# Kernel tuning notes

Measured on AMD Instinct MI355X. Metric: run time of the kernel, lower is better.

## Reference

```python
import jax, jax.numpy as jnp
import numpy as np

N_NODES = 10000
N_EDGES = 640000
DIM = 128


def setup_inputs() -> dict:
    key = jax.random.key(0)
    ks = jax.random.split(key, 10)
    s = 1.0 / np.sqrt(DIM)
    return {
        "x": jax.random.normal(ks[0], (N_NODES, DIM), dtype=jnp.float32),
        "edge_index": jax.random.randint(ks[1], (2, N_EDGES), 0, N_NODES, dtype=jnp.int64),
        "fc_w": jax.random.normal(ks[2], (DIM, DIM), dtype=jnp.float32) * s,
        "fc_b": jax.random.normal(ks[3], (DIM,), dtype=jnp.float32) * s,
        "f_lw": jax.random.normal(ks[4], (DIM, DIM), dtype=jnp.float32) * s,
        "f_lb": jax.random.normal(ks[5], (DIM,), dtype=jnp.float32) * s,
        "f_rw": jax.random.normal(ks[6], (DIM, DIM), dtype=jnp.float32) * s,
        "n_lw": jax.random.normal(ks[7], (DIM, DIM), dtype=jnp.float32) * s,
        "n_lb": jax.random.normal(ks[8], (DIM,), dtype=jnp.float32) * s,
        "n_rw": jax.random.normal(ks[9], (DIM, DIM), dtype=jnp.float32) * s,
    }


def _sage_conv(h, src, dst, lw, lb, rw, n_nodes):
    # mean aggregation of source-node features at target nodes
    msg = h[src]                                                   # [E, D]
    summed = jax.ops.segment_sum(msg, dst, num_segments=n_nodes)   # [N, D]
    cnt = jax.ops.segment_sum(jnp.ones_like(dst, dtype=h.dtype), dst, num_segments=n_nodes)
    agg = summed / jnp.maximum(cnt, 1.0)[:, None]
    # PyG SAGEConv: lin_l(agg) + lin_r(x); lin_l has bias, lin_r does not
    return agg @ lw.T + lb + h @ rw.T


def reference(x, edge_index, fc_w, fc_b, f_lw, f_lb, f_rw, n_lw, n_lb, n_rw):
    n_nodes = x.shape[0]
    src, dst = edge_index[0], edge_index[1]
    inp = x @ fc_w.T + fc_b                                        # fc residual branch
    h = jax.nn.relu(_sage_conv(x, src, dst, f_lw, f_lb, f_rw, n_nodes))
    # dropout(p=0.3) is identity in eval mode
    h = _sage_conv(h, src, dst, n_lw, n_lb, n_rw, n_nodes)
    return jax.nn.relu(h + inp)
```

## Files before the change

### kernel.cpp

```cpp
#include <hip/hip_runtime.h>
#include <hip/hip_fp8.h>

#define NN 10000
#define NE 640000
#define DIM 128
#define NB 157
#define REGCAP 4608
#define MT1 157
#define EPB 4096
#define G_FILL 157
#define NODECAP 128

typedef __attribute__((ext_vector_type(8))) short bf16x8;
typedef __attribute__((ext_vector_type(4))) float f32x4;

__device__ __forceinline__ unsigned short f2bf(float f) {
    unsigned u = __float_as_uint(f);
    u += 0x7FFFu + ((u >> 16) & 1u);
    return (unsigned short)(u >> 16);
}
__device__ __forceinline__ float bf2f(unsigned short h) {
    return __uint_as_float(((unsigned)h) << 16);
}
__device__ __forceinline__ unsigned char f2f8(float f) {
    __hip_fp8_e4m3 t(f);
    return (unsigned char)t.__x;
}
__device__ __forceinline__ float f82f(unsigned char u) {
    __hip_fp8_e4m3 t;
    t.__x = (__hip_fp8_storage_t)u;
    return (float)t;
}

__global__ __launch_bounds__(256) void prep_k(
        const float* __restrict__ w0, const float* __restrict__ w1,
        const float* __restrict__ w2, const float* __restrict__ w3,
        const float* __restrict__ w4,
        unsigned short* __restrict__ wb, int* __restrict__ gcur) {
    int t = blockIdx.x * 256 + threadIdx.x;
    if (t < 256) gcur[t] = 0;
    int plane = t >> 14;
    int i = t & 16383;
    const float* wp = (plane == 0) ? w0 : (plane == 1) ? w1 :
                      (plane == 2) ? w2 : (plane == 3) ? w3 : w4;
    wb[t] = f2bf(wp[i]);
}

__global__ __launch_bounds__(256) void mega1_k(
        const float* __restrict__ A,
        const unsigned short* __restrict__ wb,
        unsigned char* __restrict__ xl8,
        float* __restrict__ xr, float* __restrict__ xc,
        const int* __restrict__ src, const int* __restrict__ dst,
        int* __restrict__ gcur, unsigned* __restrict__ region) {
    int b = blockIdx.x;
    int tid = threadIdx.x;
    if (b < G_FILL) {
        __shared__ int start[NB + 1];
        __shared__ int cur[NB];
        __shared__ int gbase[NB];
        __shared__ unsigned sorted[EPB];
        if (tid < NB + 1) start[tid] = 0;
        __syncthreads();
        int base = b * EPB;
        int nE = min(EPB, NE - base);
        unsigned pk[4][4];
        int kb[4][4];
        bool cv[4];
#pragma unroll
        for (int c = 0; c < 4; ++c) {
            int e = base + c * 1024 + tid * 4;
            cv[c] = (e < NE);
            if (cv[c]) {
                int4 s = *(const int4*)(src + e);
                int4 d = *(const int4*)(dst + e);
                pk[c][0] = ((unsigned)d.x << 16) | (unsigned)s.x;
                pk[c][1] = ((unsigned)d.y << 16) | (unsigned)s.y;
                pk[c][2] = ((unsigned)d.z << 16) | (unsigned)s.z;
                pk[c][3] = ((unsigned)d.w << 16) | (unsigned)s.w;
                kb[c][0] = d.x >> 6; kb[c][1] = d.y >> 6;
                kb[c][2] = d.z >> 6; kb[c][3] = d.w >> 6;
            }
        }
#pragma unroll
        for (int c = 0; c < 4; ++c)
            if (cv[c])
#pragma unroll
                for (int j = 0; j < 4; ++j) atomicAdd(&start[kb[c][j] + 1], 1);
        __syncthreads();
        for (int off = 1; off < NB + 1; off <<= 1) {
            int v = 0;
            if (tid <= NB && tid >= off) v = start[tid - off];
            __syncthreads();
            if (tid <= NB && tid >= off) start[tid] += v;
            __syncthreads();
        }
        if (tid < NB) cur[tid] = start[tid];
        __syncthreads();
#pragma unroll
        for (int c = 0; c < 4; ++c)
            if (cv[c])
#pragma unroll
                for (int j = 0; j < 4; ++j) {
                    int q = atomicAdd(&cur[kb[c][j]], 1);
                    sorted[q] = pk[c][j];
                }
        __syncthreads();
        if (tid < NB) {
            int len = start[tid + 1] - start[tid];
            gbase[tid] = (len > 0) ? atomicAdd(&gcur[tid], len) : 0;
        }
        __syncthreads();
        for (int i = tid; i < nE; i += 256) {
            unsigned e = sorted[i];
            int bb = (int)(e >> 16) >> 6;
            int rel = gbase[bb] + (i - start[bb]);
            if (rel < REGCAP) region[(size_t)bb * REGCAP + rel] = e;
        }
        return;
    }
    int gb = b - G_FILL;
    int plane = gb / MT1;
    int mt = gb % MT1;
    const unsigned short* W = wb + (size_t)plane * (DIM * DIM);
    int lane = tid & 63;
    int wv = tid >> 6;
    int mr = lane & 15, q = lane >> 4;
    int m0 = mt * 64 + wv * 16;
    int mc = min(m0 + mr, NN - 1);

    bf16x8 afr[4];
#pragma unroll
    for (int kc = 0; kc < 4; ++kc) {
        const float* ap = A + (size_t)mc * DIM + kc * 32 + q * 8;
        float4 v0 = *(const float4*)ap;
        float4 v1 = *(const float4*)(ap + 4);
        bf16x8 f;
        f[0] = (short)f2bf(v0.x); f[1] = (short)f2bf(v0.y);
        f[2] = (short)f2bf(v0.z); f[3] = (short)f2bf(v0.w);
        f[4] = (short)f2bf(v1.x); f[5] = (short)f2bf(v1.y);
        f[6] = (short)f2bf(v1.z); f[7] = (short)f2bf(v1.w);
        afr[kc] = f;
    }
    f32x4 acc[8];
#pragma unroll
    for (int nt = 0; nt < 8; ++nt) acc[nt] = (f32x4){0.f, 0.f, 0.f, 0.f};
#pragma unroll
    for (int nt = 0; nt < 8; ++nt) {
        const unsigned short* wp = W + (size_t)(nt * 16 + mr) * DIM;
#pragma unroll
        for (int kc = 0; kc < 4; ++kc) {
            bf16x8 wfr = *(const bf16x8*)(const void*)(wp + kc * 32 + q * 8);
            acc[nt] = __builtin_amdgcn_mfma_f32_16x16x32_bf16(afr[kc], wfr, acc[nt], 0, 0, 0);
        }
    }
#pragma unroll
    for (int r = 0; r < 4; ++r) {
        int ms = m0 + q * 4 + r;
        if (ms >= NN) continue;
        if (plane == 0) {
#pragma unroll
            for (int nt = 0; nt < 8; ++nt)
                xl8[(size_t)ms * DIM + nt * 16 + mr] = f2f8(acc[nt][r]);
        } else {
            float* o = (plane == 1) ? xr : xc;
#pragma unroll
            for (int nt = 0; nt < 8; ++nt)
                o[(size_t)ms * DIM + nt * 16 + mr] = acc[nt][r];
        }
    }
}

template<int MODE>
__global__ __launch_bounds__(256) void agg_k(
        const unsigned char* __restrict__ g8,
        const float* __restrict__ xr, const float* __restrict__ b0v,
        const int* __restrict__ gcur, const unsigned* __restrict__ region,
        unsigned short* __restrict__ outb, unsigned char* __restrict__ out8) {
    int blk = blockIdx.x;
    int b = blk >> 2, sub = blk & 3;
    int n0 = b * 64 + sub * 16;
    int tid = threadIdx.x;
    __shared__ unsigned short list[16][NODECAP];
    __shared__ int cnt[16];
    if (tid < 16) cnt[tid] = 0;
    __syncthreads();
    int R = min(gcur[b], REGCAP);
    const unsigned* reg = region + (size_t)b * REGCAP;
    for (int i = tid; i < R; i += 256) {
        unsigned e = reg[i];
        int nl = (int)(e >> 16) - n0;
        if ((unsigned)nl < 16u) {
            int slot = atomicAdd(&cnt[nl], 1);
            if (slot < NODECAP) list[nl][slot] = (unsigned short)(e & 0xFFFFu);
        }
    }
    __syncthreads();

    int g = tid >> 4, d8 = tid & 15;
    int node = n0 + g;
    if (node >= NN) return;
    int trueDeg = cnt[g];
    int deg = min(trueDeg, NODECAP);
    float a[8];
#pragma unroll
    for (int j = 0; j < 8; ++j) a[j] = 0.f;
    union U { uint2 v; unsigned char c[8]; };
    int r = 0;
    for (; r + 8 <= deg; r += 8) {
        U u[8];
#pragma unroll
        for (int t = 0; t < 8; ++t) {
            int i0 = list[g][r + t];
            u[t].v = *(const uint2*)(const void*)(g8 + (size_t)i0 * DIM + d8 * 8);
        }
#pragma unroll
        for (int t = 0; t < 8; ++t)
#pragma unroll
            for (int j = 0; j < 8; ++j) a[j] += f82f(u[t].c[j]);
    }
    for (; r < deg; ++r) {
        int i0 = list[g][r];
        U u0;
        u0.v = *(const uint2*)(const void*)(g8 + (size_t)i0 * DIM + d8 * 8);
#pragma unroll
        for (int j = 0; j < 8; ++j) a[j] += f82f(u0.c[j]);
    }
    float inv = 1.f / fmaxf((float)trueDeg, 1.f);
    union B { int4 v; unsigned short us[8]; } o;
    if (MODE == 0) {
        const float* xp = xr + (size_t)node * DIM + d8 * 8;
        float4 r0 = *(const float4*)xp;
        float4 r1 = *(const float4*)(xp + 4);
        const float* bp = b0v + d8 * 8;
        float4 c0 = *(const float4*)bp;
        float4 c1 = *(const float4*)(bp + 4);
        float rv[8] = {r0.x, r0.y, r0.z, r0.w, r1.x, r1.y, r1.z, r1.w};
        float bv[8] = {c0.x, c0.y, c0.z, c0.w, c1.x, c1.y, c1.z, c1.w};
        U o8;
#pragma unroll
        for (int j = 0; j < 8; ++j) {
            float v = fmaxf(a[j] * inv + rv[j] + bv[j], 0.f);
            o.us[j] = f2bf(v);
            o8.c[j] = f2f8(v);
        }
        *(int4*)(void*)(outb + (size_t)node * DIM + d8 * 8) = o.v;
        *(uint2*)(void*)(out8 + (size_t)node * DIM + d8 * 8) = o8.v;
    } else {
#pragma unroll
        for (int j = 0; j < 8; ++j) o.us[j] = f2bf(a[j] * inv);
        *(int4*)(void*)(outb + (size_t)node * DIM + d8 * 8) = o.v;
    }
}

__global__ __launch_bounds__(128) void mega2_k(
        const unsigned short* __restrict__ m1b,
        const unsigned short* __restrict__ h1b,
        const unsigned short* __restrict__ wb,
        const float* __restrict__ xc,
        const float* __restrict__ nlb, const float* __restrict__ fcb,
        float* __restrict__ out) {
    const unsigned short* W0 = wb + (size_t)3 * DIM * DIM;
    const unsigned short* W1 = wb + (size_t)4 * DIM * DIM;
    int lane = threadIdx.x & 63;
    int wv = threadIdx.x >> 6;
    int mr = lane & 15, q = lane >> 4;
    int m0 = (int)blockIdx.x * 32 + wv * 16;
    int mc = min(m0 + mr, NN - 1);

    bf16x8 a0[4], a1[4];
#pragma unroll
    for (int kc = 0; kc < 4; ++kc) {
        a0[kc] = *(const bf16x8*)(const void*)(m1b + (size_t)mc * DIM + kc * 32 + q * 8);
        a1[kc] = *(const bf16x8*)(const void*)(h1b + (size_t)mc * DIM + kc * 32 + q * 8);
    }
    f32x4 acc[8];
#pragma unroll
    for (int nt = 0; nt < 8; ++nt) acc[nt] = (f32x4){0.f, 0.f, 0.f, 0.f};
#pragma unroll
    for (int nt = 0; nt < 8; ++nt) {
        const unsigned short* w0p = W0 + (size_t)(nt * 16 + mr) * DIM;
        const unsigned short* w1p = W1 + (size_t)(nt * 16 + mr) * DIM;
#pragma unroll
        for (int kc = 0; kc < 4; ++kc) {
            bf16x8 wf0 = *(const bf16x8*)(const void*)(w0p + kc * 32 + q * 8);
            acc[nt] = __builtin_amdgcn_mfma_f32_16x16x32_bf16(a0[kc], wf0, acc[nt], 0, 0, 0);
            bf16x8 wf1 = *(const bf16x8*)(const void*)(w1p + kc * 32 + q * 8);
            acc[nt] = __builtin_amdgcn_mfma_f32_16x16x32_bf16(a1[kc], wf1, acc[nt], 0, 0, 0);
        }
    }
    float bias[8];
#pragma unroll
    for (int nt = 0; nt < 8; ++nt) {
        int col = nt * 16 + mr;
        bias[nt] = nlb[col] + fcb[col];
    }
#pragma unroll
    for (int r = 0; r < 4; ++r) {
        int ms = m0 + q * 4 + r;
        if (ms >= NN) continue;
#pragma unroll
        for (int nt = 0; nt < 8; ++nt) {
            int col = nt * 16 + mr;
            float v = acc[nt][r] + xc[(size_t)ms * DIM + col] + bias[nt];
            out[(size_t)ms * DIM + col] = fmaxf(v, 0.f);
        }
    }
}

extern "C" void kernel_launch(void* const* d_in, const int* in_sizes, int n_in,
                              void* d_out, int out_size, void* d_ws, size_t ws_size,
                              hipStream_t stream) {
    const float* x    = (const float*)d_in[0];
    const int*   edge = (const int*)d_in[1];
    const float* fc_w = (const float*)d_in[2];
    const float* fc_b = (const float*)d_in[3];
    const float* f_lw = (const float*)d_in[4];
    const float* f_lb = (const float*)d_in[5];
    const float* f_rw = (const float*)d_in[6];
    const float* n_lw = (const float*)d_in[7];
    const float* n_lb = (const float*)d_in[8];
    const float* n_rw = (const float*)d_in[9];
    float* out = (float*)d_out;

    const int* src = edge;
    const int* dst = edge + NE;

    char* p = (char*)d_ws;
    float* xr = (float*)p;                     p += (size_t)NN * DIM * sizeof(float);
    float* xc = (float*)p;                     p += (size_t)NN * DIM * sizeof(float);
    unsigned short* h1b = (unsigned short*)p;  p += (size_t)NN * DIM * sizeof(unsigned short);
    unsigned short* m1b = (unsigned short*)p;  p += (size_t)NN * DIM * sizeof(unsigned short);
    unsigned short* wb  = (unsigned short*)p;  p += (size_t)5 * DIM * DIM * sizeof(unsigned short);
    unsigned char* xl8  = (unsigned char*)p;   p += (size_t)NN * DIM;
    unsigned char* h18  = (unsigned char*)p;   p += (size_t)NN * DIM;
    int* gcur = (int*)p;                       p += (size_t)256 * sizeof(int);
    unsigned* region = (unsigned*)p;

    prep_k<<<(5 * DIM * DIM) / 256, 256, 0, stream>>>(f_lw, f_rw, fc_w, n_lw, n_rw, wb, gcur);
    mega1_k<<<G_FILL + 3 * MT1, 256, 0, stream>>>(
        x, wb, xl8, xr, xc, src, dst, gcur, region);
    agg_k<0><<<4 * NB, 256, 0, stream>>>(xl8, xr, f_lb, gcur, region, h1b, h18);
    agg_k<1><<<4 * NB, 256, 0, stream>>>(h18, nullptr, nullptr, gcur, region, m1b, nullptr);
    mega2_k<<<2 * MT1, 128, 0, stream>>>(m1b, h1b, wb, xc, n_lb, fc_b, out);
}
```

Baseline: 144.8 us.

## Fuse second aggregation into final GEMM and use 16-node edge buckets

Edges are now bucketed by dst>>4 into 625 regions instead of 157, so each aggregation block handles exactly one 16-node bucket without rescanning a 64-node region. The first aggregation kernel saves its per-node neighbor lists and counts to global memory, and the second aggregation is fused into the final GEMM kernel, which reads those lists back and keeps the mean-aggregated rows in LDS. The weight-prep kernel is dropped: weights are converted from fp32 to bf16 on the fly inside the GEMMs, and a memset replaces the counter reset. In exchange, weight conversion is repeated per block, and the smaller region capacity of 1280 edges per bucket may overflow on skewed graphs.

```diff
diff --git a/kernel.cpp b/kernel.cpp
--- a/kernel.cpp
+++ b/kernel.cpp
@@ -4,11 +4,11 @@
 #define NN 10000
 #define NE 640000
 #define DIM 128
-#define NB 157
-#define REGCAP 4608
-#define MT1 157
+#define NB2 625
+#define RC2 1280
 #define EPB 4096
 #define G_FILL 157
+#define MT1 157
 #define NODECAP 128
 
 typedef __attribute__((ext_vector_type(8))) short bf16x8;
@@ -19,9 +19,6 @@
     u += 0x7FFFu + ((u >> 16) & 1u);
     return (unsigned short)(u >> 16);
 }
-__device__ __forceinline__ float bf2f(unsigned short h) {
-    return __uint_as_float(((unsigned)h) << 16);
-}
 __device__ __forceinline__ unsigned char f2f8(float f) {
     __hip_fp8_e4m3 t(f);
     return (unsigned char)t.__x;
@@ -31,36 +28,58 @@
     t.__x = (__hip_fp8_storage_t)u;
     return (float)t;
 }
-
-__global__ __launch_bounds__(256) void prep_k(
-        const float* __restrict__ w0, const float* __restrict__ w1,
-        const float* __restrict__ w2, const float* __restrict__ w3,
-        const float* __restrict__ w4,
-        unsigned short* __restrict__ wb, int* __restrict__ gcur) {
-    int t = blockIdx.x * 256 + threadIdx.x;
-    if (t < 256) gcur[t] = 0;
-    int plane = t >> 14;
-    int i = t & 16383;
-    const float* wp = (plane == 0) ? w0 : (plane == 1) ? w1 :
-                      (plane == 2) ? w2 : (plane == 3) ? w3 : w4;
-    wb[t] = f2bf(wp[i]);
-}
-
-__global__ __launch_bounds__(256) void mega1_k(
-        const float* __restrict__ A,
-        const unsigned short* __restrict__ wb,
-        unsigned char* __restrict__ xl8,
-        float* __restrict__ xr, float* __restrict__ xc,
+__device__ __forceinline__ bf16x8 cvt8(const float* p) {
+    float4 v0 = *(const float4*)p;
+    float4 v1 = *(const float4*)(p + 4);
+    bf16x8 f;
+    f[0] = (short)f2bf(v0.x); f[1] = (short)f2bf(v0.y);
+    f[2] = (short)f2bf(v0.z); f[3] = (short)f2bf(v0.w);
+    f[4] = (short)f2bf(v1.x); f[5] = (short)f2bf(v1.y);
+    f[6] = (short)f2bf(v1.z); f[7] = (short)f2bf(v1.w);
+    return f;
+}
+
+__device__ __forceinline__ void gather8(const unsigned char* __restrict__ g8,
+                                        const unsigned short* lst,
+                                        int deg, int d8, float* a) {
+#pragma unroll
+    for (int j = 0; j < 8; ++j) a[j] = 0.f;
+    union U { uint2 v; unsigned char c[8]; };
+    int r = 0;
+    for (; r + 8 <= deg; r += 8) {
+        U u[8];
+#pragma unroll
+        for (int t = 0; t < 8; ++t)
+            u[t].v = *(const uint2*)(const void*)(g8 + (size_t)lst[r + t] * DIM + d8 * 8);
+#pragma unroll
+        for (int t = 0; t < 8; ++t)
+#pragma unroll
+            for (int j = 0; j < 8; ++j) a[j] += f82f(u[t].c[j]);
+    }
+    for (; r < deg; ++r) {
+        U u0;
+        u0.v = *(const uint2*)(const void*)(g8 + (size_t)lst[r] * DIM + d8 * 8);
+#pragma unroll
+        for (int j = 0; j < 8; ++j) a[j] += f82f(u0.c[j]);
+    }
+}
+
+__global__ __launch_bounds__(256) void k1_k(
+        const float* __restrict__ x,
         const int* __restrict__ src, const int* __restrict__ dst,
+        const float* __restrict__ f_lw, const float* __restrict__ f_rw,
+        const float* __restrict__ fc_w,
+        unsigned char* __restrict__ xl8, float* __restrict__ xr, float* __restrict__ xc,
         int* __restrict__ gcur, unsigned* __restrict__ region) {
-    int b = blockIdx.x;
-    int tid = threadIdx.x;
+    __shared__ int start[NB2 + 1];
+    __shared__ int cur[NB2];
+    __shared__ int gbase[NB2];
+    __shared__ int tsum[256];
+    __shared__ unsigned sorted[EPB];
+    const int b = blockIdx.x;
+    const int tid = threadIdx.x;
     if (b < G_FILL) {
-        __shared__ int start[NB + 1];
-        __shared__ int cur[NB];
-        __shared__ int gbase[NB];
-        __shared__ unsigned sorted[EPB];
-        if (tid < NB + 1) start[tid] = 0;
+        for (int i = tid; i < NB2 + 1; i += 256) start[i] = 0;
         __syncthreads();
         int base = b * EPB;
         int nE = min(EPB, NE - base);
@@ -72,14 +91,14 @@
             int e = base + c * 1024 + tid * 4;
             cv[c] = (e < NE);
             if (cv[c]) {
-                int4 s = *(const int4*)(src + e);
-                int4 d = *(const int4*)(dst + e);
-                pk[c][0] = ((unsigned)d.x << 16) | (unsigned)s.x;
-                pk[c][1] = ((unsigned)d.y << 16) | (unsigned)s.y;
-                pk[c][2] = ((unsigned)d.z << 16) | (unsigned)s.z;
-                pk[c][3] = ((unsigned)d.w << 16) | (unsigned)s.w;
-                kb[c][0] = d.x >> 6; kb[c][1] = d.y >> 6;
-                kb[c][2] = d.z >> 6; kb[c][3] = d.w >> 6;
+                int4 s4 = *(const int4*)(src + e);
+                int4 d4 = *(const int4*)(dst + e);
+                pk[c][0] = ((unsigned)d4.x << 16) | (unsigned)s4.x;
+                pk[c][1] = ((unsigned)d4.y << 16) | (unsigned)s4.y;
+                pk[c][2] = ((unsigned)d4.z << 16) | (unsigned)s4.z;
+                pk[c][3] = ((unsigned)d4.w << 16) | (unsigned)s4.w;
+                kb[c][0] = d4.x >> 4; kb[c][1] = d4.y >> 4;
+                kb[c][2] = d4.z >> 4; kb[c][3] = d4.w >> 4;
             }
         }
 #pragma unroll
@@ -88,14 +107,32 @@
 #pragma unroll
                 for (int j = 0; j < 4; ++j) atomicAdd(&start[kb[c][j] + 1], 1);
         __syncthreads();
-        for (int off = 1; off < NB + 1; off <<= 1) {
-            int v = 0;
-            if (tid <= NB && tid >= off) v = start[tid - off];
+        {
+            int s = 0;
+            int i0 = 1 + tid * 3;
+#pragma unroll
+            for (int k = 0; k < 3; ++k) {
+                int idx = i0 + k;
+                if (idx < NB2 + 1) s += start[idx];
+            }
+            tsum[tid] = s;
             __syncthreads();
-            if (tid <= NB && tid >= off) start[tid] += v;
-            __syncthreads();
-        }
-        if (tid < NB) cur[tid] = start[tid];
+            for (int off = 1; off < 256; off <<= 1) {
+                int v = 0;
+                if (tid >= off) v = tsum[tid - off];
+                __syncthreads();
+                tsum[tid] += v;
+                __syncthreads();
+            }
+            int run = (tid == 0) ? 0 : tsum[tid - 1];
+#pragma unroll
+            for (int k = 0; k < 3; ++k) {
+                int idx = i0 + k;
+                if (idx < NB2 + 1) { run += start[idx]; start[idx] = run; }
+            }
+        }
+        __syncthreads();
+        for (int i = tid; i < NB2; i += 256) cur[i] = start[i];
         __syncthreads();
 #pragma unroll
         for (int c = 0; c < 4; ++c)
@@ -106,51 +143,40 @@
                     sorted[q] = pk[c][j];
                 }
         __syncthreads();
-        if (tid < NB) {
-            int len = start[tid + 1] - start[tid];
-            gbase[tid] = (len > 0) ? atomicAdd(&gcur[tid], len) : 0;
+        for (int i = tid; i < NB2; i += 256) {
+            int len = start[i + 1] - start[i];
+            gbase[i] = (len > 0) ? atomicAdd(&gcur[i], len) : 0;
         }
         __syncthreads();
         for (int i = tid; i < nE; i += 256) {
             unsigned e = sorted[i];
-            int bb = (int)(e >> 16) >> 6;
+            int bb = (int)(e >> 16) >> 4;
             int rel = gbase[bb] + (i - start[bb]);
-            if (rel < REGCAP) region[(size_t)bb * REGCAP + rel] = e;
+            if (rel < RC2) region[(size_t)bb * RC2 + rel] = e;
         }
         return;
     }
-    int gb = b - G_FILL;
-    int plane = gb / MT1;
-    int mt = gb % MT1;
-    const unsigned short* W = wb + (size_t)plane * (DIM * DIM);
-    int lane = tid & 63;
-    int wv = tid >> 6;
+    int jj = b - G_FILL;
+    int plane = jj / MT1;
+    int mt = jj - plane * MT1;
+    const float* W = (plane == 0) ? f_lw : (plane == 1) ? f_rw : fc_w;
+    int lane = tid & 63, wv = tid >> 6;
     int mr = lane & 15, q = lane >> 4;
     int m0 = mt * 64 + wv * 16;
     int mc = min(m0 + mr, NN - 1);
-
     bf16x8 afr[4];
 #pragma unroll
-    for (int kc = 0; kc < 4; ++kc) {
-        const float* ap = A + (size_t)mc * DIM + kc * 32 + q * 8;
-        float4 v0 = *(const float4*)ap;
-        float4 v1 = *(const float4*)(ap + 4);
-        bf16x8 f;
-        f[0] = (short)f2bf(v0.x); f[1] = (short)f2bf(v0.y);
-        f[2] = (short)f2bf(v0.z); f[3] = (short)f2bf(v0.w);
-        f[4] = (short)f2bf(v1.x); f[5] = (short)f2bf(v1.y);
-        f[6] = (short)f2bf(v1.z); f[7] = (short)f2bf(v1.w);
-        afr[kc] = f;
-    }
+    for (int kc = 0; kc < 4; ++kc)
+        afr[kc] = cvt8(x + (size_t)mc * DIM + kc * 32 + q * 8);
     f32x4 acc[8];
 #pragma unroll
     for (int nt = 0; nt < 8; ++nt) acc[nt] = (f32x4){0.f, 0.f, 0.f, 0.f};
 #pragma unroll
     for (int nt = 0; nt < 8; ++nt) {
-        const unsigned short* wp = W + (size_t)(nt * 16 + mr) * DIM;
+        const float* wp = W + (size_t)(nt * 16 + mr) * DIM;
 #pragma unroll
         for (int kc = 0; kc < 4; ++kc) {
-            bf16x8 wfr = *(const bf16x8*)(const void*)(wp + kc * 32 + q * 8);
+            bf16x8 wfr = cvt8(wp + kc * 32 + q * 8);
             acc[nt] = __builtin_amdgcn_mfma_f32_16x16x32_bf16(afr[kc], wfr, acc[nt], 0, 0, 0);
         }
     }
@@ -171,22 +197,21 @@
     }
 }
 
-template<int MODE>
-__global__ __launch_bounds__(256) void agg_k(
-        const unsigned char* __restrict__ g8,
-        const float* __restrict__ xr, const float* __restrict__ b0v,
+__global__ __launch_bounds__(256) void k2_k(
+        const unsigned char* __restrict__ xl8, const float* __restrict__ xr,
+        const float* __restrict__ f_lb,
         const int* __restrict__ gcur, const unsigned* __restrict__ region,
-        unsigned short* __restrict__ outb, unsigned char* __restrict__ out8) {
-    int blk = blockIdx.x;
-    int b = blk >> 2, sub = blk & 3;
-    int n0 = b * 64 + sub * 16;
-    int tid = threadIdx.x;
+        unsigned short* __restrict__ h1b, unsigned char* __restrict__ h18,
+        unsigned short* __restrict__ glist, int* __restrict__ gcnt) {
+    __shared__ int cnt[16];
     __shared__ unsigned short list[16][NODECAP];
-    __shared__ int cnt[16];
+    const int b = blockIdx.x;
+    const int tid = threadIdx.x;
     if (tid < 16) cnt[tid] = 0;
     __syncthreads();
-    int R = min(gcur[b], REGCAP);
-    const unsigned* reg = region + (size_t)b * REGCAP;
+    const int n0 = b * 16;
+    const int R = min(gcur[b], RC2);
+    const unsigned* reg = region + (size_t)b * RC2;
     for (int i = tid; i < R; i += 256) {
         unsigned e = reg[i];
         int nl = (int)(e >> 16) - n0;
@@ -196,113 +221,102 @@
         }
     }
     __syncthreads();
-
-    int g = tid >> 4, d8 = tid & 15;
-    int node = n0 + g;
-    if (node >= NN) return;
-    int trueDeg = cnt[g];
-    int deg = min(trueDeg, NODECAP);
+    {
+        const int4* ls = (const int4*)&list[0][0];
+        int4* gd = (int4*)(void*)(glist + (size_t)b * (16 * NODECAP));
+        gd[tid] = ls[tid];
+        if (tid < 16) gcnt[n0 + tid] = cnt[tid];
+    }
+    const int g = tid >> 4, d8 = tid & 15;
+    const int node = n0 + g;
+    const int trueDeg = cnt[g];
+    const int deg = min(trueDeg, NODECAP);
     float a[8];
-#pragma unroll
-    for (int j = 0; j < 8; ++j) a[j] = 0.f;
-    union U { uint2 v; unsigned char c[8]; };
-    int r = 0;
-    for (; r + 8 <= deg; r += 8) {
-        U u[8];
-#pragma unroll
-        for (int t = 0; t < 8; ++t) {
-            int i0 = list[g][r + t];
-            u[t].v = *(const uint2*)(const void*)(g8 + (size_t)i0 * DIM + d8 * 8);
-        }
-#pragma unroll
-        for (int t = 0; t < 8; ++t)
-#pragma unroll
-            for (int j = 0; j < 8; ++j) a[j] += f82f(u[t].c[j]);
-    }
-    for (; r < deg; ++r) {
-        int i0 = list[g][r];
-        U u0;
-        u0.v = *(const uint2*)(const void*)(g8 + (size_t)i0 * DIM + d8 * 8);
-#pragma unroll
-        for (int j = 0; j < 8; ++j) a[j] += f82f(u0.c[j]);
-    }
+    gather8(xl8, &list[g][0], deg, d8, a);
     float inv = 1.f / fmaxf((float)trueDeg, 1.f);
+    const float* xp = xr + (size_t)node * DIM + d8 * 8;
+    float4 r0 = *(const float4*)xp;
+    float4 r1 = *(const float4*)(xp + 4);
+    const float* bp = f_lb + d8 * 8;
+    float4 c0 = *(const float4*)bp;
+    float4 c1 = *(const float4*)(bp + 4);
+    float rv[8] = {r0.x, r0.y, r0.z, r0.w, r1.x, r1.y, r1.z, r1.w};
+    float bv[8] = {c0.x, c0.y, c0.z, c0.w, c1.x, c1.y, c1.z, c1.w};
     union B { int4 v; unsigned short us[8]; } o;
-    if (MODE == 0) {
-        const float* xp = xr + (size_t)node * DIM + d8 * 8;
-        float4 r0 = *(const float4*)xp;
-        float4 r1 = *(const float4*)(xp + 4);
-        const float* bp = b0v + d8 * 8;
-        float4 c0 = *(const float4*)bp;
-        float4 c1 = *(const float4*)(bp + 4);
-        float rv[8] = {r0.x, r0.y, r0.z, r0.w, r1.x, r1.y, r1.z, r1.w};
-        float bv[8] = {c0.x, c0.y, c0.z, c0.w, c1.x, c1.y, c1.z, c1.w};
-        U o8;
-#pragma unroll
-        for (int j = 0; j < 8; ++j) {
-            float v = fmaxf(a[j] * inv + rv[j] + bv[j], 0.f);
-            o.us[j] = f2bf(v);
-            o8.c[j] = f2f8(v);
-        }
-        *(int4*)(void*)(outb + (size_t)node * DIM + d8 * 8) = o.v;
-        *(uint2*)(void*)(out8 + (size_t)node * DIM + d8 * 8) = o8.v;
-    } else {
-#pragma unroll
-        for (int j = 0; j < 8; ++j) o.us[j] = f2bf(a[j] * inv);
-        *(int4*)(void*)(outb + (size_t)node * DIM + d8 * 8) = o.v;
-    }
-}
-
-__global__ __launch_bounds__(128) void mega2_k(
-        const unsigned short* __restrict__ m1b,
-        const unsigned short* __restrict__ h1b,
-        const unsigned short* __restrict__ wb,
+    union U8 { uint2 v; unsigned char c[8]; } o8;
+#pragma unroll
+    for (int j = 0; j < 8; ++j) {
+        float v = fmaxf(a[j] * inv + rv[j] + bv[j], 0.f);
+        o.us[j] = f2bf(v);
+        o8.c[j] = f2f8(v);
+    }
+    *(int4*)(void*)(h1b + (size_t)node * DIM + d8 * 8) = o.v;
+    *(uint2*)(void*)(h18 + (size_t)node * DIM + d8 * 8) = o8.v;
+}
+
+__global__ __launch_bounds__(256) void k3_k(
+        const unsigned char* __restrict__ h18, const unsigned short* __restrict__ h1b,
+        const float* __restrict__ n_lw, const float* __restrict__ n_rw,
+        const float* __restrict__ n_lb, const float* __restrict__ fc_b,
         const float* __restrict__ xc,
-        const float* __restrict__ nlb, const float* __restrict__ fcb,
+        const unsigned short* __restrict__ glist, const int* __restrict__ gcnt,
         float* __restrict__ out) {
-    const unsigned short* W0 = wb + (size_t)3 * DIM * DIM;
-    const unsigned short* W1 = wb + (size_t)4 * DIM * DIM;
-    int lane = threadIdx.x & 63;
-    int wv = threadIdx.x >> 6;
-    int mr = lane & 15, q = lane >> 4;
-    int m0 = (int)blockIdx.x * 32 + wv * 16;
-    int mc = min(m0 + mr, NN - 1);
-
+    __shared__ int cnt[16];
+    __shared__ unsigned short list[16][NODECAP];
+    __shared__ unsigned short m1t[16][DIM];
+    const int b = blockIdx.x;
+    const int tid = threadIdx.x;
+    {
+        int4* ls = (int4*)&list[0][0];
+        const int4* gs = (const int4*)(const void*)(glist + (size_t)b * (16 * NODECAP));
+        ls[tid] = gs[tid];
+        if (tid < 16) cnt[tid] = gcnt[b * 16 + tid];
+    }
+    __syncthreads();
+    const int g = tid >> 4, d8 = tid & 15;
+    const int trueDeg = cnt[g];
+    const int deg = min(trueDeg, NODECAP);
+    float a[8];
+    gather8(h18, &list[g][0], deg, d8, a);
+    float inv = 1.f / fmaxf((float)trueDeg, 1.f);
+    union B { int4 v; unsigned short us[8]; } mo;
+#pragma unroll
+    for (int j = 0; j < 8; ++j) mo.us[j] = f2bf(a[j] * inv);
+    *(int4*)(void*)(&m1t[g][d8 * 8]) = mo.v;
+    __syncthreads();
+    const int lane = tid & 63, wv = tid >> 6;
+    const int mr = lane & 15, q = lane >> 4;
+    const int m0 = b * 16;
     bf16x8 a0[4], a1[4];
 #pragma unroll
     for (int kc = 0; kc < 4; ++kc) {
-        a0[kc] = *(const bf16x8*)(const void*)(m1b + (size_t)mc * DIM + kc * 32 + q * 8);
-        a1[kc] = *(const bf16x8*)(const void*)(h1b + (size_t)mc * DIM + kc * 32 + q * 8);
-    }
-    f32x4 acc[8];
-#pragma unroll
-    for (int nt = 0; nt < 8; ++nt) acc[nt] = (f32x4){0.f, 0.f, 0.f, 0.f};
-#pragma unroll
-    for (int nt = 0; nt < 8; ++nt) {
-        const unsigned short* w0p = W0 + (size_t)(nt * 16 + mr) * DIM;
-        const unsigned short* w1p = W1 + (size_t)(nt * 16 + mr) * DIM;
+        a0[kc] = *(const bf16x8*)(const void*)(&m1t[mr][kc * 32 + q * 8]);
+        a1[kc] = *(const bf16x8*)(const void*)(h1b + (size_t)(m0 + mr) * DIM + kc * 32 + q * 8);
+    }
+    f32x4 acc[2];
+    acc[0] = (f32x4){0.f, 0.f, 0.f, 0.f};
+    acc[1] = (f32x4){0.f, 0.f, 0.f, 0.f};
+#pragma unroll
+    for (int ntl = 0; ntl < 2; ++ntl) {
+        int nt = wv * 2 + ntl;
+        const float* w0p = n_lw + (size_t)(nt * 16 + mr) * DIM;
+        const float* w1p = n_rw + (size_t)(nt * 16 + mr) * DIM;
 #pragma unroll
         for (int kc = 0; kc < 4; ++kc) {
-            bf16x8 wf0 = *(const bf16x8*)(const void*)(w0p + kc * 32 + q * 8);
-            acc[nt] = __builtin_amdgcn_mfma_f32_16x16x32_bf16(a0[kc], wf0, acc[nt], 0, 0, 0);
-            bf16x8 wf1 = *(const bf16x8*)(const void*)(w1p + kc * 32 + q * 8);
-            acc[nt] = __builtin_amdgcn_mfma_f32_16x16x32_bf16(a1[kc], wf1, acc[nt], 0, 0, 0);
-        }
-    }
-    float bias[8];
-#pragma unroll
-    for (int nt = 0; nt < 8; ++nt) {
-        int col = nt * 16 + mr;
-        bias[nt] = nlb[col] + fcb[col];
-    }
-#pragma unroll
-    for (int r = 0; r < 4; ++r) {
-        int ms = m0 + q * 4 + r;
-        if (ms >= NN) continue;
-#pragma unroll
-        for (int nt = 0; nt < 8; ++nt) {
-            int col = nt * 16 + mr;
-            float v = acc[nt][r] + xc[(size_t)ms * DIM + col] + bias[nt];
+            bf16x8 wf0 = cvt8(w0p + kc * 32 + q * 8);
+            acc[ntl] = __builtin_amdgcn_mfma_f32_16x16x32_bf16(a0[kc], wf0, acc[ntl], 0, 0, 0);
+            bf16x8 wf1 = cvt8(w1p + kc * 32 + q * 8);
+            acc[ntl] = __builtin_amdgcn_mfma_f32_16x16x32_bf16(a1[kc], wf1, acc[ntl], 0, 0, 0);
+        }
+    }
+#pragma unroll
+    for (int ntl = 0; ntl < 2; ++ntl) {
+        int col = (wv * 2 + ntl) * 16 + mr;
+        float bias = n_lb[col] + fc_b[col];
+#pragma unroll
+        for (int r = 0; r < 4; ++r) {
+            int ms = m0 + q * 4 + r;
+            float v = acc[ntl][r] + xc[(size_t)ms * DIM + col] + bias;
             out[(size_t)ms * DIM + col] = fmaxf(v, 0.f);
         }
     }
@@ -327,20 +341,19 @@
     const int* dst = edge + NE;
 
     char* p = (char*)d_ws;
-    float* xr = (float*)p;                     p += (size_t)NN * DIM * sizeof(float);
-    float* xc = (float*)p;                     p += (size_t)NN * DIM * sizeof(float);
-    unsigned short* h1b = (unsigned short*)p;  p += (size_t)NN * DIM * sizeof(unsigned short);
-    unsigned short* m1b = (unsigned short*)p;  p += (size_t)NN * DIM * sizeof(unsigned short);
-    unsigned short* wb  = (unsigned short*)p;  p += (size_t)5 * DIM * DIM * sizeof(unsigned short);
-    unsigned char* xl8  = (unsigned char*)p;   p += (size_t)NN * DIM;
-    unsigned char* h18  = (unsigned char*)p;   p += (size_t)NN * DIM;
-    int* gcur = (int*)p;                       p += (size_t)256 * sizeof(int);
+    float* xr = (float*)p;                    p += (size_t)NN * DIM * sizeof(float);
+    float* xc = (float*)p;                    p += (size_t)NN * DIM * sizeof(float);
+    unsigned short* h1b = (unsigned short*)p; p += (size_t)NN * DIM * sizeof(unsigned short);
+    unsigned char* xl8 = (unsigned char*)p;   p += (size_t)NN * DIM;
+    unsigned char* h18 = (unsigned char*)p;   p += (size_t)NN * DIM;
+    unsigned short* glist = (unsigned short*)p; p += (size_t)NB2 * 16 * NODECAP * sizeof(unsigned short);
+    int* gcnt = (int*)p;                      p += (size_t)NN * sizeof(int);
+    int* gcur = (int*)p;                      p += 4096;
     unsigned* region = (unsigned*)p;
 
-    prep_k<<<(5 * DIM * DIM) / 256, 256, 0, stream>>>(f_lw, f_rw, fc_w, n_lw, n_rw, wb, gcur);
-    mega1_k<<<G_FILL + 3 * MT1, 256, 0, stream>>>(
-        x, wb, xl8, xr, xc, src, dst, gcur, region);
-    agg_k<0><<<4 * NB, 256, 0, stream>>>(xl8, xr, f_lb, gcur, region, h1b, h18);
-    agg_k<1><<<4 * NB, 256, 0, stream>>>(h18, nullptr, nullptr, gcur, region, m1b, nullptr);
-    mega2_k<<<2 * MT1, 128, 0, stream>>>(m1b, h1b, wb, xc, n_lb, fc_b, out);
-}
+    hipMemsetAsync(gcur, 0, NB2 * sizeof(int), stream);
+    k1_k<<<G_FILL + 3 * MT1, 256, 0, stream>>>(
+        x, src, dst, f_lw, f_rw, fc_w, xl8, xr, xc, gcur, region);
+    k2_k<<<NB2, 256, 0, stream>>>(xl8, xr, f_lb, gcur, region, h1b, h18, glist, gcnt);
+    k3_k<<<NB2, 256, 0, stream>>>(h18, h1b, n_lw, n_rw, n_lb, fc_b, xc, glist, gcnt, out);
+}
```

New measurement: 143.3 us. Within noise of the previous version (-1.1%).
